# Kernel tuning notes

Measured on AMD Instinct MI355X. Metric: run time of the kernel, lower is better.

Reference implementation:

```python
import jax, jax.numpy as jnp
import numpy as np
import math

N_LAYERS = 6
F = 512   # num_feature
H = 8     # num_head
DH = F // H
V = 32000 # vocab size
B = 64
S = 512   # == PositionalEncoding max_len
EPS = 1e-5


def _make_pe(max_len, d_model):
    position = np.arange(max_len, dtype=np.float32)[:, None]
    div_term = np.exp(np.arange(0, d_model, 2, dtype=np.float32) * (-math.log(10000.0) / d_model))
    pe = np.zeros((max_len, d_model), dtype=np.float32)
    pe[:, 0::2] = np.sin(position * div_term)
    pe[:, 1::2] = np.cos(position * div_term)
    return jnp.asarray(pe)


def setup_inputs() -> dict:
    key = jax.random.key(0)
    ks = jax.random.split(key, 16)
    w = lambda k, shape, s=0.02: (jax.random.normal(k, shape, dtype=jnp.float32) * s)
    inp = {
        "text": jax.random.randint(ks[0], (B, S), 0, V),
        "emb": jax.random.normal(ks[1], (V, F), dtype=jnp.float32) * 0.25,
        "pe": _make_pe(S, F),
        # per-layer params stacked on leading N axis
        "Wq": w(ks[2], (N_LAYERS, F, F)), "bq": jnp.zeros((N_LAYERS, F), jnp.float32),
        "Wk": w(ks[3], (N_LAYERS, F, F)), "bk": jnp.zeros((N_LAYERS, F), jnp.float32),
        "Wv": w(ks[4], (N_LAYERS, F, F)), "bv": jnp.zeros((N_LAYERS, F), jnp.float32),
        "g1": jnp.ones((N_LAYERS, F), jnp.float32), "beta1": jnp.zeros((N_LAYERS, F), jnp.float32),
        "Wf": w(ks[5], (N_LAYERS, F, F)), "bf": jnp.zeros((N_LAYERS, F), jnp.float32),
        "g2": jnp.ones((N_LAYERS, F), jnp.float32), "beta2": jnp.zeros((N_LAYERS, F), jnp.float32),
    }
    return inp


def _layernorm(x, g, b):
    m = jnp.mean(x, axis=-1, keepdims=True)
    v = jnp.mean(jnp.square(x - m), axis=-1, keepdims=True)
    return (x - m) * jax.lax.rsqrt(v + EPS) * g + b


def _encoder_layer(x, Wq, bq, Wk, bk, Wv, bv, g1, beta1, Wf, bf, g2, beta2):
    Bz, Sz, Fz = x.shape
    q = (x @ Wq + bq).reshape(Bz, Sz, H, DH)
    k = (x @ Wk + bk).reshape(Bz, Sz, H, DH)
    v = (x @ Wv + bv).reshape(Bz, Sz, H, DH)
    # FAITHFUL to source bug: attention over HEADS per token, no 1/sqrt(d) scaling.
    score = jnp.einsum('bshd,bsgd->bshg', q, k)          # [B,S,H,H]
    weight = jax.nn.softmax(score, axis=-1)
    attn = jnp.einsum('bshg,bsgd->bshd', weight, v).reshape(Bz, Sz, Fz)
    x = _layernorm(attn + x, g1, beta1)
    x = _layernorm((x @ Wf + bf) + x, g2, beta2)
    return x


def reference(text, emb, pe, Wq, bq, Wk, bk, Wv, bv, g1, beta1, Wf, bf, g2, beta2):
    x = emb[text] + pe[None, :text.shape[1], :]  # embedding + pos-enc (dropout = eval identity)
    for i in range(N_LAYERS):
        x = _encoder_layer(x, Wq[i], bq[i], Wk[i], bk[i], Wv[i], bv[i],
                           g1[i], beta1[i], Wf[i], bf[i], g2[i], beta2[i])
    return x
```

## Files before the change

kernel.cpp:

```cpp
#include <hip/hip_runtime.h>
#include <stdint.h>

typedef unsigned short u16;
using frag8 = __attribute__((ext_vector_type(8))) short;
using f32x4 = __attribute__((ext_vector_type(4))) float;

#define NTOK 32768
#define FDIM 512

__device__ __forceinline__ float bflo(uint32_t p){ union{uint32_t u; float f;} v; v.u = p<<16; return v.f; }
__device__ __forceinline__ float bfhi(uint32_t p){ union{uint32_t u; float f;} v; v.u = p & 0xffff0000u; return v.f; }
__device__ __forceinline__ float bf1(u16 x){ union{uint32_t u; float f;} v; v.u = ((uint32_t)x)<<16; return v.f; }
__device__ __forceinline__ u16 f2bf(float f){
  union{float f; uint32_t u;} v; v.f = f;
  uint32_t u = v.u;
  u += 0x7fffu + ((u>>16)&1u);
  return (u16)(u>>16);
}

__device__ __forceinline__ void async16(const void* g, void* l){
  __builtin_amdgcn_global_load_lds((const __attribute__((address_space(1))) uint32_t*)g,
                                   (__attribute__((address_space(3))) uint32_t*)l, 16, 0, 0);
}

__global__ __launch_bounds__(256) void embed_kernel(const int* __restrict__ text,
    const float* __restrict__ emb, const float* __restrict__ pe,
    u16* __restrict__ xb, const int tok0){
  const int gid = blockIdx.x*256 + threadIdx.x;
  const int base = gid*4;
  const int tl = base >> 9;
  const int f  = base & 511;
  const int tg = tl + tok0;
  const int s  = tg & 511;
  const int tok = text[tg];
  const float4 e4 = *(const float4*)(emb + (size_t)tok*FDIM + f);
  const float4 p4 = *(const float4*)(pe  + (size_t)s*FDIM + f);
  ushort4 ob;
  ob.x = f2bf(e4.x + p4.x);
  ob.y = f2bf(e4.y + p4.y);
  ob.z = f2bf(e4.z + p4.z);
  ob.w = f2bf(e4.w + p4.w);
  *(ushort4*)(xb + base) = ob;
}

__global__ __launch_bounds__(256) void transpose_w(const float* __restrict__ Wq,
    const float* __restrict__ Wk, const float* __restrict__ Wv, const float* __restrict__ Wf,
    u16* __restrict__ WT){
  const int gid = blockIdx.x*256 + threadIdx.x;
  const int n   = gid & 2047;
  const int k8  = (gid>>11) & 63;
  const int lay = gid >> 17;
  const float* src; int col;
  if      (n <  512){ src = Wq; col = n;      }
  else if (n < 1024){ src = Wk; col = n-512;  }
  else if (n < 1536){ src = Wv; col = n-1024; }
  else              { src = Wf; col = n-1536; }
  src += (size_t)lay*FDIM*FDIM;
  u16 vals[8] __attribute__((aligned(16)));
  #pragma unroll
  for (int i=0;i<8;i++) vals[i] = f2bf(src[(size_t)(k8*8+i)*FDIM + col]);
  *(int4*)(WT + ((size_t)lay*2048 + n)*FDIM + k8*8) = *(const int4*)vals;
}

template<int MODE>
__global__ __launch_bounds__(512, 2) void gemm8p(
    const u16* __restrict__ A, const u16* __restrict__ BT,
    const float* __restrict__ b0, const float* __restrict__ b1, const float* __restrict__ b2,
    const u16* __restrict__ resid, u16* __restrict__ C, const int ldC, const int NB){
  __shared__ __attribute__((aligned(16))) char lds[131072];
  const int nwg = gridDim.x;
  const int orig = blockIdx.x;
  const int wg = ((nwg & 7)==0) ? ((orig&7)*(nwg>>3) + (orig>>3)) : orig;
  const int nblk = wg % NB, mblk = wg / NB;
  const int m0 = mblk<<8, n0 = nblk<<8;
  const int tid = threadIdx.x;
  const int wid = tid>>6, l = tid&63;
  const int lm = l&15, quad = l>>4;
  const int wm = wid>>2, wn = wid&3;

  const int cg = (l&3) ^ ((l>>3)&3);
  const char* aSrc = (const char*)A  + ((size_t)(m0 + (wid>>2)*128 + (wid&3)*16 + (l>>2)))*1024 + cg*16;
  const char* bSrc = (const char*)BT + ((size_t)(n0 + (wid>>1)*64  + (wid&1)*16 + (l>>2)))*1024 + cg*16;
  char* ldsAs = lds + wid*1024;
  char* ldsBs = lds + 65536 + wid*1024;

#define STGA(kt, kw, mh) async16(aSrc + (mh)*65536 + (kt)*128 + (kw)*64, \
                                 ldsAs + (((kt)&1)*32768) + (kw)*16384 + (mh)*8192)
#define STGB(kt, kw, nh) async16(bSrc + (nh)*32768 + (kt)*128 + (kw)*64, \
                                 ldsBs + (((kt)&1)*32768) + (kw)*16384 + (nh)*8192)

  f32x4 acc[8][4];
  #pragma unroll
  for (int i=0;i<8;i++)
    #pragma unroll
    for (int j=0;j<4;j++){ f32x4 z = {0.f,0.f,0.f,0.f}; acc[i][j] = z; }

  const int csw = (quad ^ ((l>>1)&3))*16;
  const char* aRd = lds + wm*4096 + lm*64 + csw;
  const char* bRd = lds + 65536 + wn*2048 + lm*64 + csw;

  frag8 a[4][2], bR[2][2][2];

  STGA(0,0,0); STGA(0,1,0); STGB(0,0,0); STGB(0,1,0); STGB(0,0,1); STGB(0,1,1); STGA(0,0,1); STGA(0,1,1);
  STGA(1,0,0); STGA(1,1,0); STGB(1,0,0); STGB(1,1,0); STGB(1,0,1); STGB(1,1,1);
  asm volatile("s_waitcnt vmcnt(6)" ::: "memory");
  __builtin_amdgcn_s_barrier();

#define RDA(BUF, MH) { _Pragma("unroll") for (int mi_=0;mi_<4;mi_++){ \
    a[mi_][0] = *(const frag8*)(aRd + (BUF)*32768 + (MH)*8192 + mi_*1024); \
    a[mi_][1] = *(const frag8*)(aRd + (BUF)*32768 + 16384 + (MH)*8192 + mi_*1024); } }
#define RDB(BUF, NH) { _Pragma("unroll") for (int nj_=0;nj_<2;nj_++){ \
    bR[NH][nj_][0] = *(const frag8*)(bRd + (BUF)*32768 + (NH)*8192 + nj_*1024); \
    bR[NH][nj_][1] = *(const frag8*)(bRd + (BUF)*32768 + 16384 + (NH)*8192 + nj_*1024); } }
#define MM(MH, NH) { __builtin_amdgcn_s_setprio(1); \
  _Pragma("unroll") for (int kw_=0;kw_<2;kw_++) \
  _Pragma("unroll") for (int mi_=0;mi_<4;mi_++) \
  _Pragma("unroll") for (int nj_=0;nj_<2;nj_++) \
    acc[(MH)*4+mi_][(NH)*2+nj_] = __builtin_amdgcn_mfma_f32_16x16x32_bf16( \
        a[mi_][kw_], bR[NH][nj_][kw_], acc[(MH)*4+mi_][(NH)*2+nj_], 0,0,0); \
  __builtin_amdgcn_s_setprio(0); }
#define BAR __builtin_amdgcn_s_barrier()

#define ITER(T, FULL) { \
   RDA(((T)&1),0); RDB(((T)&1),0); STGA((T)+1,0,1); STGA((T)+1,1,1); \
           BAR; MM(0,0); BAR; \
   RDB(((T)&1),1); if (FULL){ STGA((T)+2,0,0); STGA((T)+2,1,0); } \
           BAR; MM(0,1); BAR; \
   RDA(((T)&1),1); if (FULL){ STGB((T)+2,0,0); STGB((T)+2,1,0); } \
           BAR; MM(1,0); BAR; \
   if (FULL){ STGB((T)+2,0,1); STGB((T)+2,1,1); } \
           BAR; MM(1,1); \
           if (FULL){ asm volatile("s_waitcnt vmcnt(6)" ::: "memory"); } \
           else     { asm volatile("s_waitcnt vmcnt(0)" ::: "memory"); } \
           BAR; \
   RDA((((T)+1)&1),0); RDB((((T)+1)&1),0); if (FULL){ STGA((T)+2,0,1); STGA((T)+2,1,1); } \
           BAR; MM(0,0); BAR; \
   RDB((((T)+1)&1),1); if (FULL){ STGA((T)+3,0,0); STGA((T)+3,1,0); } \
           BAR; MM(0,1); BAR; \
   RDA((((T)+1)&1),1); if (FULL){ STGB((T)+3,0,0); STGB((T)+3,1,0); } \
           BAR; MM(1,0); BAR; \
   if (FULL){ STGB((T)+3,0,1); STGB((T)+3,1,1); } \
           BAR; MM(1,1); \
           if (FULL){ asm volatile("s_waitcnt vmcnt(6)" ::: "memory"); } \
           BAR; \
}

  ITER(0,1)
  ITER(2,1)
  ITER(4,1)
  ITER(6,0)

#undef ITER
#undef BAR
#undef MM
#undef RDB
#undef RDA
#undef STGB
#undef STGA

  float bias[4]; int cols[4];
  #pragma unroll
  for (int nj=0;nj<4;nj++){
    const int c = n0 + wn*64 + nj*16 + lm;
    cols[nj] = c;
    if (MODE==0) bias[nj] = (c<512 ? b0[c] : (c<1024 ? b1[c-512] : b2[c-1024]));
    else         bias[nj] = b0[c];
  }
  #pragma unroll
  for (int mi=0; mi<8; mi++){
    const int rbase = m0 + wm*128 + mi*16 + quad*4;
    #pragma unroll
    for (int r=0;r<4;r++){
      const size_t row = (size_t)(rbase + r);
      #pragma unroll
      for (int nj=0;nj<4;nj++){
        float v = acc[mi][nj][r] + bias[nj];
        if (MODE==1) v += bf1(resid[row*FDIM + cols[nj]]);
        C[row*(size_t)ldC + cols[nj]] = f2bf(v);
      }
    }
  }
}

__global__ __launch_bounds__(256) void attn_ln1(const u16* __restrict__ qkvb,
    const u16* __restrict__ xb, const float* __restrict__ gam, const float* __restrict__ bet,
    u16* __restrict__ y1b){
  __shared__ __attribute__((aligned(16))) u16 sQ[4][1536];
  __shared__ float sWt[4][64];
  const int tid = threadIdx.x, w = tid>>6, l = tid&63;
  const int t = blockIdx.x*4 + w;
  {
    const int4* src = (const int4*)(qkvb + (size_t)t*1536);
    int4* dst = (int4*)(&sQ[w][0]);
    #pragma unroll
    for (int i=0;i<3;i++) dst[i*64 + l] = src[i*64 + l];
  }
  __syncthreads();
  const int h = l>>3, g = l&7;
  const u16* qrow = &sQ[w][h*64];
  const u16* krow = &sQ[w][512 + g*64];
  float sc = 0.f;
  const int dstart = (l&31)*2;
  #pragma unroll
  for (int i=0;i<32;i++){
    const int d = (dstart + 2*i) & 63;
    const uint32_t qp = *(const uint32_t*)(qrow + d);
    const uint32_t kp = *(const uint32_t*)(krow + d);
    sc += bflo(qp)*bflo(kp) + bfhi(qp)*bfhi(kp);
  }
  float mx = sc;
  mx = fmaxf(mx, __shfl_xor(mx,1));
  mx = fmaxf(mx, __shfl_xor(mx,2));
  mx = fmaxf(mx, __shfl_xor(mx,4));
  const float e = __expf(sc - mx);
  float ssum = e;
  ssum += __shfl_xor(ssum,1);
  ssum += __shfl_xor(ssum,2);
  ssum += __shfl_xor(ssum,4);
  sWt[w][l] = e / ssum;
  __syncthreads();
  float wt[8];
  #pragma unroll
  for (int gg=0;gg<8;gg++) wt[gg] = sWt[w][h*8+gg];
  float att[8] = {0,0,0,0,0,0,0,0};
  const int d0 = (l&7)*8;
  #pragma unroll
  for (int gg=0;gg<8;gg++){
    const int4 vv = *(const int4*)(&sQ[w][1024 + gg*64 + d0]);
    const uint32_t* vp = (const uint32_t*)&vv;
    #pragma unroll
    for (int p=0;p<4;p++){
      att[2*p]   += wt[gg]*bflo(vp[p]);
      att[2*p+1] += wt[gg]*bfhi(vp[p]);
    }
  }
  const size_t rb = (size_t)t*FDIM + l*8;
  const int4 xv = *(const int4*)(xb + rb);
  const uint32_t* xp = (const uint32_t*)&xv;
  float y[8]; float s1=0.f, s2=0.f;
  #pragma unroll
  for (int p=0;p<4;p++){
    y[2*p]   = att[2*p]   + bflo(xp[p]);
    y[2*p+1] = att[2*p+1] + bfhi(xp[p]);
  }
  #pragma unroll
  for (int j=0;j<8;j++){ s1 += y[j]; s2 += y[j]*y[j]; }
  #pragma unroll
  for (int off=1; off<64; off<<=1){ s1 += __shfl_xor(s1,off); s2 += __shfl_xor(s2,off); }
  const float mean = s1*(1.f/512.f);
  const float var  = s2*(1.f/512.f) - mean*mean;
  const float rstd = rsqrtf(var + 1e-5f);
  const float4 g0 = *(const float4*)(gam + l*8);
  const float4 g1v = *(const float4*)(gam + l*8 + 4);
  const float4 b0v = *(const float4*)(bet + l*8);
  const float4 b1v = *(const float4*)(bet + l*8 + 4);
  float of[8];
  of[0]=(y[0]-mean)*rstd*g0.x + b0v.x;
  of[1]=(y[1]-mean)*rstd*g0.y + b0v.y;
  of[2]=(y[2]-mean)*rstd*g0.z + b0v.z;
  of[3]=(y[3]-mean)*rstd*g0.w + b0v.w;
  of[4]=(y[4]-mean)*rstd*g1v.x + b1v.x;
  of[5]=(y[5]-mean)*rstd*g1v.y + b1v.y;
  of[6]=(y[6]-mean)*rstd*g1v.z + b1v.z;
  of[7]=(y[7]-mean)*rstd*g1v.w + b1v.w;
  u16 ob[8] __attribute__((aligned(16)));
  #pragma unroll
  for (int j=0;j<8;j++) ob[j] = f2bf(of[j]);
  *(int4*)(y1b + rb) = *(const int4*)ob;
}

__global__ __launch_bounds__(256) void ln2_kernel(const u16* __restrict__ z,
    const float* __restrict__ gam, const float* __restrict__ bet,
    u16* __restrict__ xb, float* __restrict__ outp, const int final_){
  const int tid = threadIdx.x, w = tid>>6, l = tid&63;
  const int t = blockIdx.x*4 + w;
  const size_t rb = (size_t)t*FDIM + l*8;
  const int4 zv = *(const int4*)(z + rb);
  const uint32_t* zp = (const uint32_t*)&zv;
  float y[8];
  #pragma unroll
  for (int p=0;p<4;p++){ y[2*p]=bflo(zp[p]); y[2*p+1]=bfhi(zp[p]); }
  float s1=0.f, s2=0.f;
  #pragma unroll
  for (int j=0;j<8;j++){ s1+=y[j]; s2+=y[j]*y[j]; }
  #pragma unroll
  for (int off=1; off<64; off<<=1){ s1 += __shfl_xor(s1,off); s2 += __shfl_xor(s2,off); }
  const float mean = s1*(1.f/512.f);
  const float var  = s2*(1.f/512.f) - mean*mean;
  const float rstd = rsqrtf(var + 1e-5f);
  const float4 g0 = *(const float4*)(gam + l*8);
  const float4 g1v = *(const float4*)(gam + l*8 + 4);
  const float4 b0v = *(const float4*)(bet + l*8);
  const float4 b1v = *(const float4*)(bet + l*8 + 4);
  float of[8];
  of[0]=(y[0]-mean)*rstd*g0.x + b0v.x;
  of[1]=(y[1]-mean)*rstd*g0.y + b0v.y;
  of[2]=(y[2]-mean)*rstd*g0.z + b0v.z;
  of[3]=(y[3]-mean)*rstd*g0.w + b0v.w;
  of[4]=(y[4]-mean)*rstd*g1v.x + b1v.x;
  of[5]=(y[5]-mean)*rstd*g1v.y + b1v.y;
  of[6]=(y[6]-mean)*rstd*g1v.z + b1v.z;
  of[7]=(y[7]-mean)*rstd*g1v.w + b1v.w;
  if (final_){
    float4 o0; o0.x=of[0]; o0.y=of[1]; o0.z=of[2]; o0.w=of[3];
    float4 o1; o1.x=of[4]; o1.y=of[5]; o1.z=of[6]; o1.w=of[7];
    *(float4*)(outp + rb) = o0;
    *(float4*)(outp + rb + 4) = o1;
  } else {
    u16 ob[8] __attribute__((aligned(16)));
    #pragma unroll
    for (int j=0;j<8;j++) ob[j] = f2bf(of[j]);
    *(int4*)(xb + rb) = *(const int4*)ob;
  }
}

extern "C" void kernel_launch(void* const* d_in, const int* in_sizes, int n_in,
                              void* d_out, int out_size, void* d_ws, size_t ws_size,
                              hipStream_t stream){
  const int*   text = (const int*)d_in[0];
  const float* emb = (const float*)d_in[1];
  const float* pe  = (const float*)d_in[2];
  const float* Wq  = (const float*)d_in[3];
  const float* bq  = (const float*)d_in[4];
  const float* Wk  = (const float*)d_in[5];
  const float* bk  = (const float*)d_in[6];
  const float* Wv  = (const float*)d_in[7];
  const float* bv  = (const float*)d_in[8];
  const float* g1  = (const float*)d_in[9];
  const float* be1 = (const float*)d_in[10];
  const float* Wf  = (const float*)d_in[11];
  const float* bf_ = (const float*)d_in[12];
  const float* g2  = (const float*)d_in[13];
  const float* be2 = (const float*)d_in[14];
  float* outp = (float*)d_out;

  const size_t wtB = (size_t)6*2048*512*2;
  int T = NTOK;
  while (T > 2048 && wtB + (size_t)T*5120 > ws_size) T >>= 1;

  char* ws = (char*)d_ws;
  u16*   WT  = (u16*)ws;
  char*  act = ws + wtB;
  u16*   xb  = (u16*)act;
  u16*   y1b = (u16*)(act + (size_t)T*1024);
  u16*   qkv = (u16*)(act + (size_t)T*2048);
  u16*   zb  = qkv;

  hipLaunchKernelGGL(transpose_w, dim3(3072), dim3(256), 0, stream, Wq, Wk, Wv, Wf, WT);

  const int chunks = NTOK / T;
  for (int c = 0; c < chunks; c++){
    const int tok0 = c*T;
    hipLaunchKernelGGL(embed_kernel, dim3(T/2), dim3(256), 0, stream, text, emb, pe, xb, tok0);
    for (int lay=0; lay<6; lay++){
      const u16* WTl = WT + (size_t)lay*2048*FDIM;
      hipLaunchKernelGGL((gemm8p<0>), dim3((T/256)*6), dim3(512), 0, stream,
          xb, WTl, bq + lay*FDIM, bk + lay*FDIM, bv + lay*FDIM, (const u16*)nullptr, qkv, 1536, 6);
      hipLaunchKernelGGL(attn_ln1, dim3(T/4), dim3(256), 0, stream,
          qkv, xb, g1 + lay*FDIM, be1 + lay*FDIM, y1b);
      hipLaunchKernelGGL((gemm8p<1>), dim3((T/256)*2), dim3(512), 0, stream,
          y1b, WTl + (size_t)1536*FDIM, bf_ + lay*FDIM, (const float*)nullptr, (const float*)nullptr,
          y1b, zb, 512, 2);
      hipLaunchKernelGGL(ln2_kernel, dim3(T/4), dim3(256), 0, stream,
          zb, g2 + lay*FDIM, be2 + lay*FDIM, xb, outp + (size_t)tok0*FDIM, (lay==5)?1:0);
    }
  }
}
```

Measured before the change: 882.8 us.

## Fuse feed-forward GEMM with residual add and LayerNorm2 in one kernel

Replaces the feed-forward GEMM plus separate LN2 kernel with a single kernel. Each block computes a 64-row by full-512-column tile and reduces row statistics across waves through LDS, then writes the normalized output directly. This removes the bf16 round trip of the intermediate z tensor and one launch per layer. In exchange it uses a smaller M tile with a different double-buffered pipeline, which reloads the weight matrix once per 64 rows.

```diff
diff --git a/kernel.cpp b/kernel.cpp
--- a/kernel.cpp
+++ b/kernel.cpp
@@ -62,11 +62,10 @@
   *(int4*)(WT + ((size_t)lay*2048 + n)*FDIM + k8*8) = *(const int4*)vals;
 }
 
-template<int MODE>
 __global__ __launch_bounds__(512, 2) void gemm8p(
     const u16* __restrict__ A, const u16* __restrict__ BT,
     const float* __restrict__ b0, const float* __restrict__ b1, const float* __restrict__ b2,
-    const u16* __restrict__ resid, u16* __restrict__ C, const int ldC, const int NB){
+    u16* __restrict__ C, const int ldC, const int NB){
   __shared__ __attribute__((aligned(16))) char lds[131072];
   const int nwg = gridDim.x;
   const int orig = blockIdx.x;
@@ -163,8 +162,7 @@
   for (int nj=0;nj<4;nj++){
     const int c = n0 + wn*64 + nj*16 + lm;
     cols[nj] = c;
-    if (MODE==0) bias[nj] = (c<512 ? b0[c] : (c<1024 ? b1[c-512] : b2[c-1024]));
-    else         bias[nj] = b0[c];
+    bias[nj] = (c<512 ? b0[c] : (c<1024 ? b1[c-512] : b2[c-1024]));
   }
   #pragma unroll
   for (int mi=0; mi<8; mi++){
@@ -175,7 +173,6 @@
       #pragma unroll
       for (int nj=0;nj<4;nj++){
         float v = acc[mi][nj][r] + bias[nj];
-        if (MODE==1) v += bf1(resid[row*FDIM + cols[nj]]);
         C[row*(size_t)ldC + cols[nj]] = f2bf(v);
       }
     }
@@ -269,48 +266,127 @@
   *(int4*)(y1b + rb) = *(const int4*)ob;
 }
 
-__global__ __launch_bounds__(256) void ln2_kernel(const u16* __restrict__ z,
-    const float* __restrict__ gam, const float* __restrict__ bet,
+__global__ __launch_bounds__(512, 4) void ff_ln2(
+    const u16* __restrict__ y1, const u16* __restrict__ WTf,
+    const float* __restrict__ bfv,
+    const float* __restrict__ g2, const float* __restrict__ be2,
     u16* __restrict__ xb, float* __restrict__ outp, const int final_){
-  const int tid = threadIdx.x, w = tid>>6, l = tid&63;
-  const int t = blockIdx.x*4 + w;
-  const size_t rb = (size_t)t*FDIM + l*8;
-  const int4 zv = *(const int4*)(z + rb);
-  const uint32_t* zp = (const uint32_t*)&zv;
-  float y[8];
-  #pragma unroll
-  for (int p=0;p<4;p++){ y[2*p]=bflo(zp[p]); y[2*p+1]=bfhi(zp[p]); }
-  float s1=0.f, s2=0.f;
-  #pragma unroll
-  for (int j=0;j<8;j++){ s1+=y[j]; s2+=y[j]*y[j]; }
-  #pragma unroll
-  for (int off=1; off<64; off<<=1){ s1 += __shfl_xor(s1,off); s2 += __shfl_xor(s2,off); }
-  const float mean = s1*(1.f/512.f);
-  const float var  = s2*(1.f/512.f) - mean*mean;
-  const float rstd = rsqrtf(var + 1e-5f);
-  const float4 g0 = *(const float4*)(gam + l*8);
-  const float4 g1v = *(const float4*)(gam + l*8 + 4);
-  const float4 b0v = *(const float4*)(bet + l*8);
-  const float4 b1v = *(const float4*)(bet + l*8 + 4);
-  float of[8];
-  of[0]=(y[0]-mean)*rstd*g0.x + b0v.x;
-  of[1]=(y[1]-mean)*rstd*g0.y + b0v.y;
-  of[2]=(y[2]-mean)*rstd*g0.z + b0v.z;
-  of[3]=(y[3]-mean)*rstd*g0.w + b0v.w;
-  of[4]=(y[4]-mean)*rstd*g1v.x + b1v.x;
-  of[5]=(y[5]-mean)*rstd*g1v.y + b1v.y;
-  of[6]=(y[6]-mean)*rstd*g1v.z + b1v.z;
-  of[7]=(y[7]-mean)*rstd*g1v.w + b1v.w;
-  if (final_){
-    float4 o0; o0.x=of[0]; o0.y=of[1]; o0.z=of[2]; o0.w=of[3];
-    float4 o1; o1.x=of[4]; o1.y=of[5]; o1.z=of[6]; o1.w=of[7];
-    *(float4*)(outp + rb) = o0;
-    *(float4*)(outp + rb + 4) = o1;
-  } else {
-    u16 ob[8] __attribute__((aligned(16)));
-    #pragma unroll
-    for (int j=0;j<8;j++) ob[j] = f2bf(of[j]);
-    *(int4*)(xb + rb) = *(const int4*)ob;
+  __shared__ __attribute__((aligned(16))) char lds[81920];
+  const int m0 = blockIdx.x << 6;
+  const int tid = threadIdx.x;
+  const int wid = tid>>6, l = tid&63;
+  const int lm = l&15, quad = l>>4;
+
+  const char* aSrc = (const char*)y1 + ((size_t)(m0 + (tid>>3)))*1024 + ((tid&7) ^ ((tid>>3)&7))*16;
+  const char* bSrc = (const char*)WTf + ((size_t)(wid*16 + (l>>2)))*1024 + ((l&3) ^ ((l>>3)&3))*16;
+  char* ldsA = lds + wid*1024;
+  char* ldsB = lds + 16384 + wid*1024;
+
+#define STA(P) async16(aSrc + (P)*128, ldsA + ((P)&1)*8192)
+#define STB(T) { _Pragma("unroll") for (int r_=0;r_<4;r_++) \
+    async16(bSrc + (size_t)r_*131072 + (T)*64, ldsB + ((T)&1)*32768 + r_*8192); }
+
+  f32x4 acc[4][4];
+  #pragma unroll
+  for (int i=0;i<4;i++)
+    #pragma unroll
+    for (int j=0;j<4;j++){ f32x4 z = {0.f,0.f,0.f,0.f}; acc[i][j] = z; }
+
+  STA(0); STB(0) STB(1)
+
+#define FTL(T_, VMC, DOB, DOA) { \
+    asm volatile("s_waitcnt vmcnt(" #VMC ")" ::: "memory"); \
+    __builtin_amdgcn_s_barrier(); \
+    asm volatile("" ::: "memory"); \
+    const char* sA_ = lds + (((T_)>>1)&1)*8192; \
+    const char* sB_ = lds + 16384 + ((T_)&1)*32768; \
+    frag8 af_[4], bf_[4]; \
+    _Pragma("unroll") \
+    for (int mi_=0;mi_<4;mi_++) \
+      af_[mi_] = *(const frag8*)(sA_ + (mi_*16+lm)*128 + ((((T_)&1)*4+quad)^(lm&7))*16); \
+    _Pragma("unroll") \
+    for (int nj_=0;nj_<4;nj_++) \
+      bf_[nj_] = *(const frag8*)(sB_ + (wid*64 + nj_*16 + lm)*64 + (quad^((lm>>1)&3))*16); \
+    __builtin_amdgcn_s_setprio(1); \
+    _Pragma("unroll") \
+    for (int mi_=0;mi_<4;mi_++) \
+      _Pragma("unroll") \
+      for (int nj_=0;nj_<4;nj_++) \
+        acc[mi_][nj_] = __builtin_amdgcn_mfma_f32_16x16x32_bf16(af_[mi_], bf_[nj_], acc[mi_][nj_], 0,0,0); \
+    __builtin_amdgcn_s_setprio(0); \
+    __builtin_amdgcn_s_barrier(); \
+    if (DOB){ STB((T_)+2) } \
+    if (DOA){ STA(((T_)>>1)+1); } \
+  }
+
+  FTL(0,4,1,1)   FTL(1,5,1,0)
+  FTL(2,4,1,1)   FTL(3,5,1,0)
+  FTL(4,4,1,1)   FTL(5,5,1,0)
+  FTL(6,4,1,1)   FTL(7,5,1,0)
+  FTL(8,4,1,1)   FTL(9,5,1,0)
+  FTL(10,4,1,1)  FTL(11,5,1,0)
+  FTL(12,4,1,1)  FTL(13,5,1,0)
+  FTL(14,4,0,0)  FTL(15,0,0,0)
+#undef FTL
+#undef STB
+#undef STA
+
+  float* ln2S = (float*)lds;
+  int cols[4]; float bia[4], gg2[4], bb2[4];
+  #pragma unroll
+  for (int nj=0;nj<4;nj++){
+    const int c = wid*64 + nj*16 + lm;
+    cols[nj] = c; bia[nj] = bfv[c]; gg2[nj] = g2[c]; bb2[nj] = be2[c];
+  }
+  #pragma unroll
+  for (int mi=0;mi<4;mi++){
+    #pragma unroll
+    for (int r=0;r<4;r++){
+      const int row_l = mi*16 + quad*4 + r;
+      const size_t rg = (size_t)(m0 + row_l)*FDIM;
+      float s1 = 0.f, s2 = 0.f;
+      #pragma unroll
+      for (int nj=0;nj<4;nj++){
+        const float v = acc[mi][nj][r] + bia[nj] + bf1(y1[rg + cols[nj]]);
+        acc[mi][nj][r] = v;
+        s1 += v; s2 += v*v;
+      }
+      s1 += __shfl_xor(s1,1); s2 += __shfl_xor(s2,1);
+      s1 += __shfl_xor(s1,2); s2 += __shfl_xor(s2,2);
+      s1 += __shfl_xor(s1,4); s2 += __shfl_xor(s2,4);
+      s1 += __shfl_xor(s1,8); s2 += __shfl_xor(s2,8);
+      if (lm == 0){
+        ln2S[(row_l*8 + wid)*2]     = s1;
+        ln2S[(row_l*8 + wid)*2 + 1] = s2;
+      }
+    }
+  }
+  __syncthreads();
+  #pragma unroll
+  for (int mi=0;mi<4;mi++){
+    #pragma unroll
+    for (int r=0;r<4;r++){
+      const int row_l = mi*16 + quad*4 + r;
+      float s1t = 0.f, s2t = 0.f;
+      #pragma unroll
+      for (int w=0;w<8;w++){
+        s1t += ln2S[(row_l*8 + w)*2];
+        s2t += ln2S[(row_l*8 + w)*2 + 1];
+      }
+      const float mean = s1t*(1.f/512.f);
+      const float var  = s2t*(1.f/512.f) - mean*mean;
+      const float rstd = rsqrtf(var + 1e-5f);
+      const size_t rg = (size_t)(m0 + row_l)*FDIM;
+      if (final_){
+        #pragma unroll
+        for (int nj=0;nj<4;nj++)
+          outp[rg + cols[nj]] = (acc[mi][nj][r]-mean)*rstd*gg2[nj] + bb2[nj];
+      } else {
+        #pragma unroll
+        for (int nj=0;nj<4;nj++)
+          xb[rg + cols[nj]] = f2bf((acc[mi][nj][r]-mean)*rstd*gg2[nj] + bb2[nj]);
+      }
+    }
   }
 }
 
@@ -344,7 +420,6 @@
   u16*   xb  = (u16*)act;
   u16*   y1b = (u16*)(act + (size_t)T*1024);
   u16*   qkv = (u16*)(act + (size_t)T*2048);
-  u16*   zb  = qkv;
 
   hipLaunchKernelGGL(transpose_w, dim3(3072), dim3(256), 0, stream, Wq, Wk, Wv, Wf, WT);
 
@@ -354,15 +429,14 @@
     hipLaunchKernelGGL(embed_kernel, dim3(T/2), dim3(256), 0, stream, text, emb, pe, xb, tok0);
     for (int lay=0; lay<6; lay++){
       const u16* WTl = WT + (size_t)lay*2048*FDIM;
-      hipLaunchKernelGGL((gemm8p<0>), dim3((T/256)*6), dim3(512), 0, stream,
-          xb, WTl, bq + lay*FDIM, bk + lay*FDIM, bv + lay*FDIM, (const u16*)nullptr, qkv, 1536, 6);
+      hipLaunchKernelGGL(gemm8p, dim3((T/256)*6), dim3(512), 0, stream,
+          xb, WTl, bq + lay*FDIM, bk + lay*FDIM, bv + lay*FDIM, qkv, 1536, 6);
       hipLaunchKernelGGL(attn_ln1, dim3(T/4), dim3(256), 0, stream,
           qkv, xb, g1 + lay*FDIM, be1 + lay*FDIM, y1b);
-      hipLaunchKernelGGL((gemm8p<1>), dim3((T/256)*2), dim3(512), 0, stream,
-          y1b, WTl + (size_t)1536*FDIM, bf_ + lay*FDIM, (const float*)nullptr, (const float*)nullptr,
-          y1b, zb, 512, 2);
-      hipLaunchKernelGGL(ln2_kernel, dim3(T/4), dim3(256), 0, stream,
-          zb, g2 + lay*FDIM, be2 + lay*FDIM, xb, outp + (size_t)tok0*FDIM, (lay==5)?1:0);
+      hipLaunchKernelGGL(ff_ln2, dim3(T/64), dim3(512), 0, stream,
+          y1b, WTl + (size_t)1536*FDIM, bf_ + lay*FDIM,
+          g2 + lay*FDIM, be2 + lay*FDIM,
+          xb, outp + (size_t)tok0*FDIM, (lay==5)?1:0);
     }
   }
 }
```

New measurement: 1.000 ms. +13.3%, slower.
